# Optimization experiments

Measured on AMD Instinct MI355X. Metric: run time of the kernel, lower is better.

Reference implementation:

```python
import jax, jax.numpy as jnp
import numpy as np

ALPHA = 1.702  # sigmoid slope in clamped-GLU
LIMIT = 7.0    # clamp limit on gate/up

B, S, H, D, E, K = 2, 2048, 1024, 1024, 8, 2


def setup_inputs() -> dict:
    key = jax.random.key(0)
    ks = jax.random.split(key, 7)
    hidden_states = jax.random.normal(ks[0], (B, S, H), jnp.float32)
    router_indices = jax.random.randint(ks[1], (B * S, K), 0, E)
    routing_weights = jax.random.uniform(ks[2], (B * S, E), dtype=jnp.float32)
    gate_up_proj = jax.random.normal(ks[3], (E, H, 2 * D), jnp.float32) * 0.02
    gate_up_bias = jax.random.normal(ks[4], (E, 2 * D), jnp.float32) * 0.02
    down_proj = jax.random.normal(ks[5], (E, D, H), jnp.float32) * 0.02
    down_bias = jax.random.normal(ks[6], (E, H), jnp.float32) * 0.02
    return dict(hidden_states=hidden_states, router_indices=router_indices,
                routing_weights=routing_weights, gate_up_proj=gate_up_proj,
                gate_up_bias=gate_up_bias, down_proj=down_proj, down_bias=down_bias)


def reference(hidden_states, router_indices, routing_weights,
              gate_up_proj, gate_up_bias, down_proj, down_bias):
    batch = hidden_states.shape[0]
    hs = hidden_states.shape[-1]
    flat = hidden_states.reshape(-1, hs)  # [T, H]
    n_exp = routing_weights.shape[1]
    # index_add with possibly duplicated (token, expert) assignments == count multiplier
    counts = (router_indices[:, :, None] == jnp.arange(n_exp)[None, None, :]).sum(1)  # [T, E]
    w = routing_weights * counts.astype(flat.dtype)  # [T, E] effective combine weight

    def step(out, xs):
        wgu, bgu, wd, bd, we = xs  # wgu:[H,2D] bgu:[2D] wd:[D,H] bd:[H] we:[T]
        gu = flat @ wgu + bgu                      # [T, 2D]
        gate = jnp.minimum(gu[:, ::2], LIMIT)      # interleaved gate channels
        up = jnp.clip(gu[:, 1::2], -LIMIT, LIMIT)  # interleaved up channels
        mid = (up + 1.0) * gate * jax.nn.sigmoid(gate * ALPHA)
        y = mid @ wd + bd                          # [T, H]
        return out + y * we[:, None], None

    out0 = jnp.zeros_like(flat)
    out, _ = jax.lax.scan(step, out0, (gate_up_proj, gate_up_bias, down_proj, down_bias, w.T))
    return out.reshape(batch, -1, hs)
```

## Files before the change

kernel.cpp:

```cpp
#include <hip/hip_runtime.h>
#include <hip/hip_bf16.h>

#define AS1 __attribute__((address_space(1)))
#define AS3 __attribute__((address_space(3)))

typedef __bf16 bf16_8 __attribute__((ext_vector_type(8)));
typedef float f32x4 __attribute__((ext_vector_type(4)));

constexpr int Tn = 4096;
constexpr int Hn = 1024;
constexpr int Dn = 1024;
constexpr int En = 8;
constexpr int Sn = 8192;
constexpr int Pmax = 9216;
constexpr int MaxTiles = 72;
constexpr float kAlpha = 1.702f;
constexpr float kLimit = 7.0f;

__device__ __forceinline__ unsigned short f2bf(float x) {
  unsigned u = __builtin_bit_cast(unsigned, x);
  u = u + 0x7FFFu + ((u >> 16) & 1u);
  return (unsigned short)(u >> 16);
}

__device__ __forceinline__ void gload_lds16(const void* gp, void* lp) {
  __builtin_amdgcn_global_load_lds(
      (const AS1 unsigned int*)(unsigned long long)gp,
      (AS3 unsigned int*)(unsigned int)(unsigned long long)lp,
      16, 0, 0);
}

__global__ void k_cvt_x(const float* __restrict__ x, unsigned short* __restrict__ xb) {
  int i = blockIdx.x * blockDim.x + threadIdx.x;
  float4 v = reinterpret_cast<const float4*>(x)[i];
  ushort4 o;
  o.x = f2bf(v.x); o.y = f2bf(v.y); o.z = f2bf(v.z); o.w = f2bf(v.w);
  reinterpret_cast<ushort4*>(xb)[i] = o;
}

__global__ void k_t_gu(const float* __restrict__ gup, unsigned short* __restrict__ wg,
                       unsigned short* __restrict__ wu) {
  __shared__ float lg[32][33], lu[32][33];
  int e = blockIdx.z, h0 = blockIdx.y * 32, d0 = blockIdx.x * 32;
  int tx = threadIdx.x, ty0 = threadIdx.y;
  const float* src = gup + ((size_t)e * Hn + h0) * (2 * Dn) + d0 * 2;
#pragma unroll
  for (int k = 0; k < 4; k++) {
    int ty = ty0 + k * 8;
    float2 v = *reinterpret_cast<const float2*>(src + (size_t)ty * (2 * Dn) + tx * 2);
    lg[ty][tx] = v.x;  lu[ty][tx] = v.y;
  }
  __syncthreads();
  unsigned short* dg = wg + ((size_t)e * Dn + d0) * Hn + h0;
  unsigned short* du = wu + ((size_t)e * Dn + d0) * Hn + h0;
#pragma unroll
  for (int k = 0; k < 4; k++) {
    int r = ty0 + k * 8;
    dg[(size_t)r * Hn + tx] = f2bf(lg[tx][r]);
    du[(size_t)r * Hn + tx] = f2bf(lu[tx][r]);
  }
}

__global__ void k_t_dn(const float* __restrict__ dwn, unsigned short* __restrict__ wdt) {
  __shared__ float ls[32][33];
  int e = blockIdx.z, d0 = blockIdx.y * 32, h0 = blockIdx.x * 32;
  int tx = threadIdx.x, ty0 = threadIdx.y;
  const float* src = dwn + ((size_t)e * Dn + d0) * Hn + h0;
#pragma unroll
  for (int k = 0; k < 4; k++) { int ty = ty0 + k * 8; ls[ty][tx] = src[(size_t)ty * Hn + tx]; }
  __syncthreads();
  unsigned short* dst = wdt + ((size_t)e * Hn + h0) * Dn + d0;
#pragma unroll
  for (int k = 0; k < 4; k++) { int r = ty0 + k * 8; dst[(size_t)r * Dn + tx] = f2bf(ls[tx][r]); }
}

__global__ void k_route(const int* __restrict__ ridx,
                        int* __restrict__ tix, int* __restrict__ pos,
                        int* __restrict__ tileE, int* __restrict__ tileP0,
                        int* __restrict__ ntiles) {
  __shared__ int lh[256][8];
  __shared__ int eoff[8];
  int tid = threadIdx.x;
#pragma unroll
  for (int e = 0; e < 8; e++) lh[tid][e] = 0;
  int myE[32];
#pragma unroll
  for (int s = 0; s < 32; s++) {
    int e = ridx[tid * 32 + s];
    myE[s] = e;
    lh[tid][e]++;
  }
  __syncthreads();
  if (tid < 8) {
    int tot = 0;
#pragma unroll 1
    for (int t = 0; t < 256; t++) { int v = lh[t][tid]; lh[t][tid] = tot; tot += v; }
    eoff[tid] = tot;
  }
  __syncthreads();
  if (tid == 0) {
    int off = 0, nt = 0;
#pragma unroll 1
    for (int e = 0; e < 8; e++) {
      int cnt = eoff[e];
      eoff[e] = off;
      int nt128 = (cnt + 127) >> 7;
      for (int k = 0; k < nt128; k++) { tileE[nt] = e; tileP0[nt] = off + k * 128; nt++; }
      off += nt128 * 128;
    }
    *ntiles = nt;
  }
  __syncthreads();
  for (int p = tid; p < Pmax; p += 256) tix[p] = 0;
  __syncthreads();
#pragma unroll
  for (int s = 0; s < 32; s++) {
    int slot = tid * 32 + s;
    int e = myE[s];
    int p = eoff[e] + (lh[tid][e]++);
    pos[slot] = p;
    tix[p] = slot >> 1;
  }
}

__launch_bounds__(256, 2)
__global__ void k_gemm1(const unsigned short* __restrict__ xb,
                        const unsigned short* __restrict__ wg,
                        const unsigned short* __restrict__ wu,
                        const float* __restrict__ gub,
                        const int* __restrict__ tix,
                        const int* __restrict__ tileE,
                        const int* __restrict__ tileP0,
                        const int* __restrict__ ntiles,
                        unsigned short* __restrict__ midc) {
  constexpr int BM = 128, BN = 64, BK = 64;
  if ((int)blockIdx.x >= *ntiles) return;
  __shared__ __align__(16) unsigned short Xs[BM * BK];
  __shared__ __align__(16) unsigned short Gs[BN * BK];
  __shared__ __align__(16) unsigned short Us[BN * BK];
  const int e = tileE[blockIdx.x];
  const int p0 = tileP0[blockIdx.x];
  const int n0 = blockIdx.y * BN;
  const int tid = threadIdx.x;
  const int wv = tid >> 6, lane = tid & 63;
  const int wr = wv >> 1, wc = wv & 1;
  const int r8 = lane >> 3, c8 = lane & 7;

  int tokc[4];
#pragma unroll
  for (int c = 0; c < 4; c++) tokc[c] = tix[p0 + (c * 4 + wv) * 8 + r8];

  const unsigned short* Gp = wg + ((size_t)e * Dn + n0) * Hn;
  const unsigned short* Up = wu + ((size_t)e * Dn + n0) * Hn;

  f32x4 ag[4][2], au[4][2];
#pragma unroll
  for (int i = 0; i < 4; i++)
#pragma unroll
    for (int j = 0; j < 2; j++) { ag[i][j] = f32x4{0.f,0.f,0.f,0.f}; au[i][j] = f32x4{0.f,0.f,0.f,0.f}; }

  for (int k0 = 0; k0 < Hn; k0 += BK) {
#pragma unroll
    for (int c = 0; c < 4; c++) {
      int ch = c * 4 + wv;
      gload_lds16(xb + (size_t)tokc[c] * Hn + k0 + c8 * 8, (void*)(Xs + ch * 512));
    }
#pragma unroll
    for (int c = 0; c < 2; c++) {
      int ch = c * 4 + wv;
      gload_lds16(Gp + (size_t)(ch * 8 + r8) * Hn + k0 + c8 * 8, (void*)(Gs + ch * 512));
      gload_lds16(Up + (size_t)(ch * 8 + r8) * Hn + k0 + c8 * 8, (void*)(Us + ch * 512));
    }
    asm volatile("s_waitcnt vmcnt(0)" ::: "memory");
    __syncthreads();
    const int fr = lane & 15, kg = lane >> 4;
#pragma unroll
    for (int kk = 0; kk < 2; kk++) {
      bf16_8 a[4], bg[2], bu[2];
#pragma unroll
      for (int i = 0; i < 4; i++)
        a[i] = *reinterpret_cast<const bf16_8*>(Xs + (wr * 64 + i * 16 + fr) * BK + kk * 32 + kg * 8);
#pragma unroll
      for (int j = 0; j < 2; j++) {
        bg[j] = *reinterpret_cast<const bf16_8*>(Gs + (wc * 32 + j * 16 + fr) * BK + kk * 32 + kg * 8);
        bu[j] = *reinterpret_cast<const bf16_8*>(Us + (wc * 32 + j * 16 + fr) * BK + kk * 32 + kg * 8);
      }
#pragma unroll
      for (int i = 0; i < 4; i++)
#pragma unroll
        for (int j = 0; j < 2; j++) {
          ag[i][j] = __builtin_amdgcn_mfma_f32_16x16x32_bf16(a[i], bg[j], ag[i][j], 0, 0, 0);
          au[i][j] = __builtin_amdgcn_mfma_f32_16x16x32_bf16(a[i], bu[j], au[i][j], 0, 0, 0);
        }
    }
    __syncthreads();
  }

  const int fr = lane & 15, rg = lane >> 4;
#pragma unroll
  for (int i = 0; i < 4; i++) {
#pragma unroll
    for (int r = 0; r < 4; r++) {
      int row = p0 + wr * 64 + i * 16 + rg * 4 + r;
#pragma unroll
      for (int j = 0; j < 2; j++) {
        int d = n0 + wc * 32 + j * 16 + fr;
        float g = ag[i][j][r] + gub[e * 2 * Dn + 2 * d];
        float u = au[i][j][r] + gub[e * 2 * Dn + 2 * d + 1];
        g = fminf(g, kLimit);
        u = fminf(fmaxf(u, -kLimit), kLimit);
        float sg = 1.0f / (1.0f + __expf(-kAlpha * g));
        float mid = (u + 1.0f) * g * sg;
        midc[(size_t)row * Dn + d] = f2bf(mid);
      }
    }
  }
}

__launch_bounds__(256, 2)
__global__ void k_gemm2(const unsigned short* __restrict__ midc,
                        const unsigned short* __restrict__ wdt,
                        const int* __restrict__ tileE,
                        const int* __restrict__ tileP0,
                        const int* __restrict__ ntiles,
                        float* __restrict__ ys) {
  constexpr int BM = 128, BN = 64, BK = 64;
  if ((int)blockIdx.x >= *ntiles) return;
  __shared__ __align__(16) unsigned short As[BM * BK];
  __shared__ __align__(16) unsigned short Bs[BN * BK];
  const int e = tileE[blockIdx.x];
  const int p0 = tileP0[blockIdx.x];
  const int n0 = blockIdx.y * BN;
  const int tid = threadIdx.x;
  const int wv = tid >> 6, lane = tid & 63;
  const int wr = wv >> 1, wc = wv & 1;
  const int r8 = lane >> 3, c8 = lane & 7;
  const unsigned short* Ap = midc + (size_t)p0 * Dn;
  const unsigned short* Bp = wdt + ((size_t)e * Hn + n0) * Dn;

  f32x4 acc[4][2];
#pragma unroll
  for (int i = 0; i < 4; i++)
#pragma unroll
    for (int j = 0; j < 2; j++) acc[i][j] = f32x4{0.f,0.f,0.f,0.f};

  for (int k0 = 0; k0 < Dn; k0 += BK) {
#pragma unroll
    for (int c = 0; c < 4; c++) {
      int ch = c * 4 + wv;
      gload_lds16(Ap + (size_t)(ch * 8 + r8) * Dn + k0 + c8 * 8, (void*)(As + ch * 512));
    }
#pragma unroll
    for (int c = 0; c < 2; c++) {
      int ch = c * 4 + wv;
      gload_lds16(Bp + (size_t)(ch * 8 + r8) * Dn + k0 + c8 * 8, (void*)(Bs + ch * 512));
    }
    asm volatile("s_waitcnt vmcnt(0)" ::: "memory");
    __syncthreads();
    const int fr = lane & 15, kg = lane >> 4;
#pragma unroll
    for (int kk = 0; kk < 2; kk++) {
      bf16_8 a[4], b[2];
#pragma unroll
      for (int i = 0; i < 4; i++)
        a[i] = *reinterpret_cast<const bf16_8*>(As + (wr * 64 + i * 16 + fr) * BK + kk * 32 + kg * 8);
#pragma unroll
      for (int j = 0; j < 2; j++)
        b[j] = *reinterpret_cast<const bf16_8*>(Bs + (wc * 32 + j * 16 + fr) * BK + kk * 32 + kg * 8);
#pragma unroll
      for (int i = 0; i < 4; i++)
#pragma unroll
        for (int j = 0; j < 2; j++)
          acc[i][j] = __builtin_amdgcn_mfma_f32_16x16x32_bf16(a[i], b[j], acc[i][j], 0, 0, 0);
    }
    __syncthreads();
  }

  const int fr = lane & 15, rg = lane >> 4;
#pragma unroll
  for (int i = 0; i < 4; i++)
#pragma unroll
    for (int r = 0; r < 4; r++) {
      int row = p0 + wr * 64 + i * 16 + rg * 4 + r;
#pragma unroll
      for (int j = 0; j < 2; j++) {
        int col = n0 + wc * 32 + j * 16 + fr;
        ys[(size_t)row * Hn + col] = acc[i][j][r];
      }
    }
}

__global__ void k_combine(const float* __restrict__ ys, const int* __restrict__ ridx,
                          const float* __restrict__ rw, const int* __restrict__ pos,
                          const float* __restrict__ db, float* __restrict__ out) {
  int t = blockIdx.x;
  int h0 = threadIdx.x * 4;
  int e0 = ridx[2 * t], e1 = ridx[2 * t + 1];
  int p0 = pos[2 * t], p1 = pos[2 * t + 1];
  float w0 = rw[t * En + e0], w1 = rw[t * En + e1];
  float4 y0 = *reinterpret_cast<const float4*>(ys + (size_t)p0 * Hn + h0);
  float4 y1 = *reinterpret_cast<const float4*>(ys + (size_t)p1 * Hn + h0);
  float4 b0 = *reinterpret_cast<const float4*>(db + (size_t)e0 * Hn + h0);
  float4 b1 = *reinterpret_cast<const float4*>(db + (size_t)e1 * Hn + h0);
  float4 o;
  o.x = w0 * (y0.x + b0.x) + w1 * (y1.x + b1.x);
  o.y = w0 * (y0.y + b0.y) + w1 * (y1.y + b1.y);
  o.z = w0 * (y0.z + b0.z) + w1 * (y1.z + b1.z);
  o.w = w0 * (y0.w + b0.w) + w1 * (y1.w + b1.w);
  *reinterpret_cast<float4*>(out + (size_t)t * Hn + h0) = o;
}

extern "C" void kernel_launch(void* const* d_in, const int* in_sizes, int n_in,
                              void* d_out, int out_size, void* d_ws, size_t ws_size,
                              hipStream_t stream) {
  (void)in_sizes; (void)n_in; (void)out_size; (void)ws_size;
  const float* hs  = (const float*)d_in[0];
  const int*   ri  = (const int*)d_in[1];
  const float* rw  = (const float*)d_in[2];
  const float* gup = (const float*)d_in[3];
  const float* gub = (const float*)d_in[4];
  const float* dwn = (const float*)d_in[5];
  const float* db  = (const float*)d_in[6];
  float* out = (float*)d_out;

  char* ws = (char*)d_ws;
  int* tix    = (int*)(ws);
  int* pos    = (int*)(ws + 65536);
  int* tileE  = (int*)(ws + 131072);
  int* tileP0 = (int*)(ws + 131584);
  int* ntiles = (int*)(ws + 132096);
  unsigned short* xb   = (unsigned short*)(ws + 262144);
  unsigned short* wg   = (unsigned short*)(ws + 262144 + 8388608);
  unsigned short* wu   = (unsigned short*)(ws + 262144 + 8388608 + 16777216);
  unsigned short* wdt  = (unsigned short*)(ws + 262144 + 8388608 + 2*16777216);
  unsigned short* midc = (unsigned short*)(ws + 262144 + 8388608 + 3*16777216);
  float* ys            = (float*)(ws + 262144 + 8388608 + 3*16777216 + (size_t)Pmax * Dn * 2);

  k_route<<<dim3(1), dim3(256), 0, stream>>>(ri, tix, pos, tileE, tileP0, ntiles);
  k_cvt_x<<<dim3(Tn * Hn / 4 / 256), dim3(256), 0, stream>>>(hs, xb);
  k_t_gu<<<dim3(Dn / 32, Hn / 32, En), dim3(32, 8), 0, stream>>>(gup, wg, wu);
  k_t_dn<<<dim3(Hn / 32, Dn / 32, En), dim3(32, 8), 0, stream>>>(dwn, wdt);
  k_gemm1<<<dim3(MaxTiles, Dn / 64), dim3(256), 0, stream>>>(xb, wg, wu, gub, tix, tileE, tileP0, ntiles, midc);
  k_gemm2<<<dim3(MaxTiles, Hn / 64), dim3(256), 0, stream>>>(midc, wdt, tileE, tileP0, ntiles, ys);
  k_combine<<<dim3(Tn), dim3(256), 0, stream>>>(ys, ri, rw, pos, db, out);
}
```

Baseline: 163.1 us.

## Double-buffer GEMM loads, remap workgroups, vectorize transposes, store expert outputs in bf16

Both grouped GEMMs now double-buffer their LDS tiles and issue the loads for step t+2 while computing step t. They also raise wave priority around the MFMA block and remap workgroup IDs in a chiplet-aware order. The weight transpose kernels use wider tiles with float4 reads and 16-byte packed bf16 writes. The down-projection output is stored as bf16 rather than fp32, and the combine kernel processes 8 elements per thread. Together these aim to hide global-load latency and cut memory traffic, at the cost of more LDS use and some extra rounding of the intermediate output.

```diff
diff --git a/kernel.cpp b/kernel.cpp
--- a/kernel.cpp
+++ b/kernel.cpp
@@ -11,7 +11,6 @@
 constexpr int Hn = 1024;
 constexpr int Dn = 1024;
 constexpr int En = 8;
-constexpr int Sn = 8192;
 constexpr int Pmax = 9216;
 constexpr int MaxTiles = 72;
 constexpr float kAlpha = 1.702f;
@@ -22,6 +21,11 @@
   u = u + 0x7FFFu + ((u >> 16) & 1u);
   return (unsigned short)(u >> 16);
 }
+__device__ __forceinline__ unsigned pack2(float a, float b) {
+  return (unsigned)f2bf(a) | ((unsigned)f2bf(b) << 16);
+}
+__device__ __forceinline__ float bflo(unsigned v) { return __builtin_bit_cast(float, v << 16); }
+__device__ __forceinline__ float bfhi(unsigned v) { return __builtin_bit_cast(float, v & 0xFFFF0000u); }
 
 __device__ __forceinline__ void gload_lds16(const void* gp, void* lp) {
   __builtin_amdgcn_global_load_lds(
@@ -40,38 +44,57 @@
 
 __global__ void k_t_gu(const float* __restrict__ gup, unsigned short* __restrict__ wg,
                        unsigned short* __restrict__ wu) {
-  __shared__ float lg[32][33], lu[32][33];
-  int e = blockIdx.z, h0 = blockIdx.y * 32, d0 = blockIdx.x * 32;
-  int tx = threadIdx.x, ty0 = threadIdx.y;
-  const float* src = gup + ((size_t)e * Hn + h0) * (2 * Dn) + d0 * 2;
-#pragma unroll
-  for (int k = 0; k < 4; k++) {
-    int ty = ty0 + k * 8;
-    float2 v = *reinterpret_cast<const float2*>(src + (size_t)ty * (2 * Dn) + tx * 2);
-    lg[ty][tx] = v.x;  lu[ty][tx] = v.y;
-  }
-  __syncthreads();
-  unsigned short* dg = wg + ((size_t)e * Dn + d0) * Hn + h0;
-  unsigned short* du = wu + ((size_t)e * Dn + d0) * Hn + h0;
-#pragma unroll
-  for (int k = 0; k < 4; k++) {
-    int r = ty0 + k * 8;
-    dg[(size_t)r * Hn + tx] = f2bf(lg[tx][r]);
-    du[(size_t)r * Hn + tx] = f2bf(lu[tx][r]);
+  __shared__ float lg[32][65], lu[32][65];
+  const int e = blockIdx.z, h0 = blockIdx.y * 64, d0 = blockIdx.x * 32;
+  const int tid = threadIdx.x;
+  {
+    const int hrow = tid >> 2, q = tid & 3;
+    const float* src = gup + ((size_t)e * Hn + h0 + hrow) * (2 * Dn) + d0 * 2 + q * 16;
+#pragma unroll
+    for (int j = 0; j < 4; j++) {
+      float4 v = *reinterpret_cast<const float4*>(src + j * 4);
+      int dp = q * 8 + j * 2;
+      lg[dp][hrow] = v.x; lu[dp][hrow] = v.y;
+      lg[dp + 1][hrow] = v.z; lu[dp + 1][hrow] = v.w;
+    }
+  }
+  __syncthreads();
+  {
+    const int d = tid >> 3, hc = (tid & 7) * 8;
+    uint4 og, ou;
+    og.x = pack2(lg[d][hc + 0], lg[d][hc + 1]); ou.x = pack2(lu[d][hc + 0], lu[d][hc + 1]);
+    og.y = pack2(lg[d][hc + 2], lg[d][hc + 3]); ou.y = pack2(lu[d][hc + 2], lu[d][hc + 3]);
+    og.z = pack2(lg[d][hc + 4], lg[d][hc + 5]); ou.z = pack2(lu[d][hc + 4], lu[d][hc + 5]);
+    og.w = pack2(lg[d][hc + 6], lg[d][hc + 7]); ou.w = pack2(lu[d][hc + 6], lu[d][hc + 7]);
+    *reinterpret_cast<uint4*>(wg + ((size_t)e * Dn + d0 + d) * Hn + h0 + hc) = og;
+    *reinterpret_cast<uint4*>(wu + ((size_t)e * Dn + d0 + d) * Hn + h0 + hc) = ou;
   }
 }
 
 __global__ void k_t_dn(const float* __restrict__ dwn, unsigned short* __restrict__ wdt) {
-  __shared__ float ls[32][33];
-  int e = blockIdx.z, d0 = blockIdx.y * 32, h0 = blockIdx.x * 32;
-  int tx = threadIdx.x, ty0 = threadIdx.y;
-  const float* src = dwn + ((size_t)e * Dn + d0) * Hn + h0;
-#pragma unroll
-  for (int k = 0; k < 4; k++) { int ty = ty0 + k * 8; ls[ty][tx] = src[(size_t)ty * Hn + tx]; }
-  __syncthreads();
-  unsigned short* dst = wdt + ((size_t)e * Hn + h0) * Dn + d0;
-#pragma unroll
-  for (int k = 0; k < 4; k++) { int r = ty0 + k * 8; dst[(size_t)r * Dn + tx] = f2bf(ls[tx][r]); }
+  __shared__ float lt[32][65];
+  const int e = blockIdx.z, h0 = blockIdx.x * 32, d0 = blockIdx.y * 64;
+  const int tid = threadIdx.x;
+  {
+    const int drow = tid >> 2, q = tid & 3;
+    const float* src = dwn + ((size_t)e * Dn + d0 + drow) * Hn + h0 + q * 8;
+#pragma unroll
+    for (int j = 0; j < 2; j++) {
+      float4 v = *reinterpret_cast<const float4*>(src + j * 4);
+      int hr = q * 8 + j * 4;
+      lt[hr][drow] = v.x; lt[hr + 1][drow] = v.y; lt[hr + 2][drow] = v.z; lt[hr + 3][drow] = v.w;
+    }
+  }
+  __syncthreads();
+  {
+    const int h = tid >> 3, dc = (tid & 7) * 8;
+    uint4 o;
+    o.x = pack2(lt[h][dc + 0], lt[h][dc + 1]);
+    o.y = pack2(lt[h][dc + 2], lt[h][dc + 3]);
+    o.z = pack2(lt[h][dc + 4], lt[h][dc + 5]);
+    o.w = pack2(lt[h][dc + 6], lt[h][dc + 7]);
+    *reinterpret_cast<uint4*>(wdt + ((size_t)e * Hn + h0 + h) * Dn + d0 + dc) = o;
+  }
 }
 
 __global__ void k_route(const int* __restrict__ ridx,
@@ -133,18 +156,24 @@
                         const int* __restrict__ tileP0,
                         const int* __restrict__ ntiles,
                         unsigned short* __restrict__ midc) {
-  constexpr int BM = 128, BN = 64, BK = 64;
-  if ((int)blockIdx.x >= *ntiles) return;
-  __shared__ __align__(16) unsigned short Xs[BM * BK];
-  __shared__ __align__(16) unsigned short Gs[BN * BK];
-  __shared__ __align__(16) unsigned short Us[BN * BK];
-  const int e = tileE[blockIdx.x];
-  const int p0 = tileP0[blockIdx.x];
-  const int n0 = blockIdx.y * BN;
+  constexpr int BM = 128, BN = 64, BK = 64, NSTEP = Hn / BK;
+  __shared__ __align__(16) unsigned short Xs[2][BM * BK];
+  __shared__ __align__(16) unsigned short Gs[2][BN * BK];
+  __shared__ __align__(16) unsigned short Us[2][BN * BK];
+  const int nwg = gridDim.x * gridDim.y;
+  const int orig = blockIdx.y * gridDim.x + blockIdx.x;
+  const int wgid = (orig & 7) * (nwg >> 3) + (orig >> 3);
+  const int bx = wgid % gridDim.x;
+  const int by = wgid / gridDim.x;
+  if (bx >= *ntiles) return;
+  const int e = tileE[bx];
+  const int p0 = tileP0[bx];
+  const int n0 = by * BN;
   const int tid = threadIdx.x;
   const int wv = tid >> 6, lane = tid & 63;
   const int wr = wv >> 1, wc = wv & 1;
   const int r8 = lane >> 3, c8 = lane & 7;
+  const int fr = lane & 15, kg = (lane >> 4) & 3;
 
   int tokc[4];
 #pragma unroll
@@ -153,50 +182,66 @@
   const unsigned short* Gp = wg + ((size_t)e * Dn + n0) * Hn;
   const unsigned short* Up = wu + ((size_t)e * Dn + n0) * Hn;
 
-  f32x4 ag[4][2], au[4][2];
-#pragma unroll
-  for (int i = 0; i < 4; i++)
-#pragma unroll
-    for (int j = 0; j < 2; j++) { ag[i][j] = f32x4{0.f,0.f,0.f,0.f}; au[i][j] = f32x4{0.f,0.f,0.f,0.f}; }
-
-  for (int k0 = 0; k0 < Hn; k0 += BK) {
+  auto stage = [&](int k0, int cur) {
 #pragma unroll
     for (int c = 0; c < 4; c++) {
       int ch = c * 4 + wv;
-      gload_lds16(xb + (size_t)tokc[c] * Hn + k0 + c8 * 8, (void*)(Xs + ch * 512));
+      gload_lds16(xb + (size_t)tokc[c] * Hn + k0 + c8 * 8, (void*)(&Xs[cur][ch * 512]));
     }
 #pragma unroll
     for (int c = 0; c < 2; c++) {
       int ch = c * 4 + wv;
-      gload_lds16(Gp + (size_t)(ch * 8 + r8) * Hn + k0 + c8 * 8, (void*)(Gs + ch * 512));
-      gload_lds16(Up + (size_t)(ch * 8 + r8) * Hn + k0 + c8 * 8, (void*)(Us + ch * 512));
-    }
-    asm volatile("s_waitcnt vmcnt(0)" ::: "memory");
-    __syncthreads();
-    const int fr = lane & 15, kg = lane >> 4;
+      gload_lds16(Gp + (size_t)(ch * 8 + r8) * Hn + k0 + c8 * 8, (void*)(&Gs[cur][ch * 512]));
+      gload_lds16(Up + (size_t)(ch * 8 + r8) * Hn + k0 + c8 * 8, (void*)(&Us[cur][ch * 512]));
+    }
+  };
+
+  f32x4 ag[4][2], au[4][2];
+#pragma unroll
+  for (int i = 0; i < 4; i++)
+#pragma unroll
+    for (int j = 0; j < 2; j++) { ag[i][j] = f32x4{0.f,0.f,0.f,0.f}; au[i][j] = f32x4{0.f,0.f,0.f,0.f}; }
+
+  stage(0, 0);
+  stage(BK, 1);
+  asm volatile("s_waitcnt vmcnt(8)" ::: "memory");
+  __builtin_amdgcn_s_barrier();
+
+  for (int t = 0; t < NSTEP; ++t) {
+    const int cur = t & 1;
+    bf16_8 a[2][4], bg[2][2], bu[2][2];
 #pragma unroll
     for (int kk = 0; kk < 2; kk++) {
-      bf16_8 a[4], bg[2], bu[2];
 #pragma unroll
       for (int i = 0; i < 4; i++)
-        a[i] = *reinterpret_cast<const bf16_8*>(Xs + (wr * 64 + i * 16 + fr) * BK + kk * 32 + kg * 8);
+        a[kk][i] = *reinterpret_cast<const bf16_8*>(&Xs[cur][(wr * 64 + i * 16 + fr) * BK + kk * 32 + kg * 8]);
 #pragma unroll
       for (int j = 0; j < 2; j++) {
-        bg[j] = *reinterpret_cast<const bf16_8*>(Gs + (wc * 32 + j * 16 + fr) * BK + kk * 32 + kg * 8);
-        bu[j] = *reinterpret_cast<const bf16_8*>(Us + (wc * 32 + j * 16 + fr) * BK + kk * 32 + kg * 8);
+        bg[kk][j] = *reinterpret_cast<const bf16_8*>(&Gs[cur][(wc * 32 + j * 16 + fr) * BK + kk * 32 + kg * 8]);
+        bu[kk][j] = *reinterpret_cast<const bf16_8*>(&Us[cur][(wc * 32 + j * 16 + fr) * BK + kk * 32 + kg * 8]);
       }
+    }
+    asm volatile("s_waitcnt lgkmcnt(0)" ::: "memory");
+    __builtin_amdgcn_s_barrier();
+    int tn = t + 2; if (tn >= NSTEP) tn -= NSTEP;
+    stage(tn * BK, cur);
+    __builtin_amdgcn_s_setprio(1);
+#pragma unroll
+    for (int kk = 0; kk < 2; kk++)
 #pragma unroll
       for (int i = 0; i < 4; i++)
 #pragma unroll
         for (int j = 0; j < 2; j++) {
-          ag[i][j] = __builtin_amdgcn_mfma_f32_16x16x32_bf16(a[i], bg[j], ag[i][j], 0, 0, 0);
-          au[i][j] = __builtin_amdgcn_mfma_f32_16x16x32_bf16(a[i], bu[j], au[i][j], 0, 0, 0);
+          ag[i][j] = __builtin_amdgcn_mfma_f32_16x16x32_bf16(a[kk][i], bg[kk][j], ag[i][j], 0, 0, 0);
+          au[i][j] = __builtin_amdgcn_mfma_f32_16x16x32_bf16(a[kk][i], bu[kk][j], au[i][j], 0, 0, 0);
         }
-    }
-    __syncthreads();
-  }
-
-  const int fr = lane & 15, rg = lane >> 4;
+    __builtin_amdgcn_s_setprio(0);
+    asm volatile("s_waitcnt vmcnt(8)" ::: "memory");
+    __builtin_amdgcn_s_barrier();
+  }
+  asm volatile("s_waitcnt vmcnt(0)" ::: "memory");
+
+  const int rg = lane >> 4;
 #pragma unroll
   for (int i = 0; i < 4; i++) {
 #pragma unroll
@@ -223,60 +268,82 @@
                         const int* __restrict__ tileE,
                         const int* __restrict__ tileP0,
                         const int* __restrict__ ntiles,
-                        float* __restrict__ ys) {
-  constexpr int BM = 128, BN = 64, BK = 64;
-  if ((int)blockIdx.x >= *ntiles) return;
-  __shared__ __align__(16) unsigned short As[BM * BK];
-  __shared__ __align__(16) unsigned short Bs[BN * BK];
-  const int e = tileE[blockIdx.x];
-  const int p0 = tileP0[blockIdx.x];
-  const int n0 = blockIdx.y * BN;
+                        unsigned short* __restrict__ ys) {
+  constexpr int BM = 128, BN = 64, BK = 64, NSTEP = Dn / BK;
+  __shared__ __align__(16) unsigned short As[2][BM * BK];
+  __shared__ __align__(16) unsigned short Bs[2][BN * BK];
+  const int nwg = gridDim.x * gridDim.y;
+  const int orig = blockIdx.y * gridDim.x + blockIdx.x;
+  const int wgid = (orig & 7) * (nwg >> 3) + (orig >> 3);
+  const int bx = wgid % gridDim.x;
+  const int by = wgid / gridDim.x;
+  if (bx >= *ntiles) return;
+  const int e = tileE[bx];
+  const int p0 = tileP0[bx];
+  const int n0 = by * BN;
   const int tid = threadIdx.x;
   const int wv = tid >> 6, lane = tid & 63;
   const int wr = wv >> 1, wc = wv & 1;
   const int r8 = lane >> 3, c8 = lane & 7;
+  const int fr = lane & 15, kg = (lane >> 4) & 3;
   const unsigned short* Ap = midc + (size_t)p0 * Dn;
   const unsigned short* Bp = wdt + ((size_t)e * Hn + n0) * Dn;
 
-  f32x4 acc[4][2];
-#pragma unroll
-  for (int i = 0; i < 4; i++)
-#pragma unroll
-    for (int j = 0; j < 2; j++) acc[i][j] = f32x4{0.f,0.f,0.f,0.f};
-
-  for (int k0 = 0; k0 < Dn; k0 += BK) {
+  auto stage = [&](int k0, int cur) {
 #pragma unroll
     for (int c = 0; c < 4; c++) {
       int ch = c * 4 + wv;
-      gload_lds16(Ap + (size_t)(ch * 8 + r8) * Dn + k0 + c8 * 8, (void*)(As + ch * 512));
+      gload_lds16(Ap + (size_t)(ch * 8 + r8) * Dn + k0 + c8 * 8, (void*)(&As[cur][ch * 512]));
     }
 #pragma unroll
     for (int c = 0; c < 2; c++) {
       int ch = c * 4 + wv;
-      gload_lds16(Bp + (size_t)(ch * 8 + r8) * Dn + k0 + c8 * 8, (void*)(Bs + ch * 512));
-    }
-    asm volatile("s_waitcnt vmcnt(0)" ::: "memory");
-    __syncthreads();
-    const int fr = lane & 15, kg = lane >> 4;
+      gload_lds16(Bp + (size_t)(ch * 8 + r8) * Dn + k0 + c8 * 8, (void*)(&Bs[cur][ch * 512]));
+    }
+  };
+
+  f32x4 acc[4][2];
+#pragma unroll
+  for (int i = 0; i < 4; i++)
+#pragma unroll
+    for (int j = 0; j < 2; j++) acc[i][j] = f32x4{0.f,0.f,0.f,0.f};
+
+  stage(0, 0);
+  stage(BK, 1);
+  asm volatile("s_waitcnt vmcnt(6)" ::: "memory");
+  __builtin_amdgcn_s_barrier();
+
+  for (int t = 0; t < NSTEP; ++t) {
+    const int cur = t & 1;
+    bf16_8 a[2][4], b[2][2];
 #pragma unroll
     for (int kk = 0; kk < 2; kk++) {
-      bf16_8 a[4], b[2];
 #pragma unroll
       for (int i = 0; i < 4; i++)
-        a[i] = *reinterpret_cast<const bf16_8*>(As + (wr * 64 + i * 16 + fr) * BK + kk * 32 + kg * 8);
+        a[kk][i] = *reinterpret_cast<const bf16_8*>(&As[cur][(wr * 64 + i * 16 + fr) * BK + kk * 32 + kg * 8]);
 #pragma unroll
       for (int j = 0; j < 2; j++)
-        b[j] = *reinterpret_cast<const bf16_8*>(Bs + (wc * 32 + j * 16 + fr) * BK + kk * 32 + kg * 8);
+        b[kk][j] = *reinterpret_cast<const bf16_8*>(&Bs[cur][(wc * 32 + j * 16 + fr) * BK + kk * 32 + kg * 8]);
+    }
+    asm volatile("s_waitcnt lgkmcnt(0)" ::: "memory");
+    __builtin_amdgcn_s_barrier();
+    int tn = t + 2; if (tn >= NSTEP) tn -= NSTEP;
+    stage(tn * BK, cur);
+    __builtin_amdgcn_s_setprio(1);
+#pragma unroll
+    for (int kk = 0; kk < 2; kk++)
 #pragma unroll
       for (int i = 0; i < 4; i++)
 #pragma unroll
         for (int j = 0; j < 2; j++)
-          acc[i][j] = __builtin_amdgcn_mfma_f32_16x16x32_bf16(a[i], b[j], acc[i][j], 0, 0, 0);
-    }
-    __syncthreads();
-  }
-
-  const int fr = lane & 15, rg = lane >> 4;
+          acc[i][j] = __builtin_amdgcn_mfma_f32_16x16x32_bf16(a[kk][i], b[kk][j], acc[i][j], 0, 0, 0);
+    __builtin_amdgcn_s_setprio(0);
+    asm volatile("s_waitcnt vmcnt(6)" ::: "memory");
+    __builtin_amdgcn_s_barrier();
+  }
+  asm volatile("s_waitcnt vmcnt(0)" ::: "memory");
+
+  const int rg = lane >> 4;
 #pragma unroll
   for (int i = 0; i < 4; i++)
 #pragma unroll
@@ -285,29 +352,36 @@
 #pragma unroll
       for (int j = 0; j < 2; j++) {
         int col = n0 + wc * 32 + j * 16 + fr;
-        ys[(size_t)row * Hn + col] = acc[i][j][r];
+        ys[(size_t)row * Hn + col] = f2bf(acc[i][j][r]);
       }
     }
 }
 
-__global__ void k_combine(const float* __restrict__ ys, const int* __restrict__ ridx,
+__global__ void k_combine(const unsigned short* __restrict__ ys, const int* __restrict__ ridx,
                           const float* __restrict__ rw, const int* __restrict__ pos,
                           const float* __restrict__ db, float* __restrict__ out) {
-  int t = blockIdx.x;
-  int h0 = threadIdx.x * 4;
+  int idx = blockIdx.x * blockDim.x + threadIdx.x;
+  int t = idx >> 7, hc = (idx & 127) << 3;
   int e0 = ridx[2 * t], e1 = ridx[2 * t + 1];
   int p0 = pos[2 * t], p1 = pos[2 * t + 1];
   float w0 = rw[t * En + e0], w1 = rw[t * En + e1];
-  float4 y0 = *reinterpret_cast<const float4*>(ys + (size_t)p0 * Hn + h0);
-  float4 y1 = *reinterpret_cast<const float4*>(ys + (size_t)p1 * Hn + h0);
-  float4 b0 = *reinterpret_cast<const float4*>(db + (size_t)e0 * Hn + h0);
-  float4 b1 = *reinterpret_cast<const float4*>(db + (size_t)e1 * Hn + h0);
-  float4 o;
-  o.x = w0 * (y0.x + b0.x) + w1 * (y1.x + b1.x);
-  o.y = w0 * (y0.y + b0.y) + w1 * (y1.y + b1.y);
-  o.z = w0 * (y0.z + b0.z) + w1 * (y1.z + b1.z);
-  o.w = w0 * (y0.w + b0.w) + w1 * (y1.w + b1.w);
-  *reinterpret_cast<float4*>(out + (size_t)t * Hn + h0) = o;
+  uint4 ya = *reinterpret_cast<const uint4*>(ys + (size_t)p0 * Hn + hc);
+  uint4 yb = *reinterpret_cast<const uint4*>(ys + (size_t)p1 * Hn + hc);
+  float4 da0 = *reinterpret_cast<const float4*>(db + (size_t)e0 * Hn + hc);
+  float4 da1 = *reinterpret_cast<const float4*>(db + (size_t)e0 * Hn + hc + 4);
+  float4 db0 = *reinterpret_cast<const float4*>(db + (size_t)e1 * Hn + hc);
+  float4 db1 = *reinterpret_cast<const float4*>(db + (size_t)e1 * Hn + hc + 4);
+  float4 o0, o1;
+  o0.x = w0 * (bflo(ya.x) + da0.x) + w1 * (bflo(yb.x) + db0.x);
+  o0.y = w0 * (bfhi(ya.x) + da0.y) + w1 * (bfhi(yb.x) + db0.y);
+  o0.z = w0 * (bflo(ya.y) + da0.z) + w1 * (bflo(yb.y) + db0.z);
+  o0.w = w0 * (bfhi(ya.y) + da0.w) + w1 * (bfhi(yb.y) + db0.w);
+  o1.x = w0 * (bflo(ya.z) + da1.x) + w1 * (bflo(yb.z) + db1.x);
+  o1.y = w0 * (bfhi(ya.z) + da1.y) + w1 * (bfhi(yb.z) + db1.y);
+  o1.z = w0 * (bflo(ya.w) + da1.z) + w1 * (bflo(yb.w) + db1.z);
+  o1.w = w0 * (bfhi(ya.w) + da1.w) + w1 * (bfhi(yb.w) + db1.w);
+  *reinterpret_cast<float4*>(out + (size_t)t * Hn + hc) = o0;
+  *reinterpret_cast<float4*>(out + (size_t)t * Hn + hc + 4) = o1;
 }
 
 extern "C" void kernel_launch(void* const* d_in, const int* in_sizes, int n_in,
@@ -334,13 +408,13 @@
   unsigned short* wu   = (unsigned short*)(ws + 262144 + 8388608 + 16777216);
   unsigned short* wdt  = (unsigned short*)(ws + 262144 + 8388608 + 2*16777216);
   unsigned short* midc = (unsigned short*)(ws + 262144 + 8388608 + 3*16777216);
-  float* ys            = (float*)(ws + 262144 + 8388608 + 3*16777216 + (size_t)Pmax * Dn * 2);
+  unsigned short* ys   = (unsigned short*)(ws + 262144 + 8388608 + 3*16777216 + (size_t)Pmax * Dn * 2);
 
   k_route<<<dim3(1), dim3(256), 0, stream>>>(ri, tix, pos, tileE, tileP0, ntiles);
   k_cvt_x<<<dim3(Tn * Hn / 4 / 256), dim3(256), 0, stream>>>(hs, xb);
-  k_t_gu<<<dim3(Dn / 32, Hn / 32, En), dim3(32, 8), 0, stream>>>(gup, wg, wu);
-  k_t_dn<<<dim3(Hn / 32, Dn / 32, En), dim3(32, 8), 0, stream>>>(dwn, wdt);
+  k_t_gu<<<dim3(Dn / 32, Hn / 64, En), dim3(256), 0, stream>>>(gup, wg, wu);
+  k_t_dn<<<dim3(Hn / 32, Dn / 64, En), dim3(256), 0, stream>>>(dwn, wdt);
   k_gemm1<<<dim3(MaxTiles, Dn / 64), dim3(256), 0, stream>>>(xb, wg, wu, gub, tix, tileE, tileP0, ntiles, midc);
   k_gemm2<<<dim3(MaxTiles, Hn / 64), dim3(256), 0, stream>>>(midc, wdt, tileE, tileP0, ntiles, ys);
-  k_combine<<<dim3(Tn), dim3(256), 0, stream>>>(ys, ri, rw, pos, db, out);
-}
+  k_combine<<<dim3(Tn * Hn / 8 / 256), dim3(256), 0, stream>>>(ys, ri, rw, pos, db, out);
+}
```

Result: slower. 170.8 us (+4.7%).
